# Kernel tuning notes

Measured on AMD Instinct MI355X. Metric: run time of the kernel, lower is better.

Reference implementation:

```python
import jax, jax.numpy as jnp
import numpy as np

NC, S, T, F, D, A = 617, 200000, 15, 5, 64, 768
E, EC, L = 1000000, 20000, 2


def setup_inputs():
    key = jax.random.key(0)
    ks = jax.random.split(key, 24)
    f = jnp.float32
    sc = 0.08
    return {
        "company_ts": jax.random.normal(ks[0], (NC, T, F), f),
        "sentence_x": jax.random.normal(ks[1], (S, A), f),
        "company_ids": jnp.arange(NC, dtype=jnp.int32),
        "ei_c2c_src": jax.random.randint(ks[2], (EC,), 0, NC),
        "ei_c2c_dst": jax.random.randint(ks[3], (EC,), 0, NC),
        "ei_s2c_src": jax.random.randint(ks[4], (E,), 0, S),
        "ei_s2c_dst": jax.random.randint(ks[5], (E,), 0, NC),
        "ei_c2s_src": jax.random.randint(ks[6], (E,), 0, NC),
        "ei_c2s_dst": jax.random.randint(ks[7], (E,), 0, S),
        "bn_gamma": jnp.ones((T,), f),
        "bn_beta": jnp.zeros((T,), f),
        "lstm_Wih0": sc * jax.random.normal(ks[8], (4 * D, 1), f),
        "lstm_Whh0": sc * jax.random.normal(ks[9], (4 * D, D), f),
        "lstm_bih0": jnp.zeros((4 * D,), f),
        "lstm_bhh0": jnp.zeros((4 * D,), f),
        "lstm_Wih1": sc * jax.random.normal(ks[10], (4 * D, D), f),
        "lstm_Whh1": sc * jax.random.normal(ks[11], (4 * D, D), f),
        "lstm_bih1": jnp.zeros((4 * D,), f),
        "lstm_bhh1": jnp.zeros((4 * D,), f),
        "fc_W": sc * jax.random.normal(ks[12], (D, D), f),
        "fc_b": jnp.zeros((D,), f),
        "comp_emb": jax.random.normal(ks[13], (NC, D), f),
        "proj_W": sc * jax.random.normal(ks[14], (D, A), f),
        "proj_b": jnp.zeros((D,), f),
        "gin_W": sc * jax.random.normal(ks[15], (L, 3, D, D), f),
        "gin_b": jnp.zeros((L, 3, D), f),
        "gin_a": 0.25 * jnp.ones((L, 3), f),  # PReLU slope, torch default init
        "cls_W": sc * jax.random.normal(ks[16], (2, D), f),
        "cls_b": jnp.zeros((2,), f),
    }


def _lstm_layer(x, Wih, Whh, bih, bhh):
    # x: [N, T, I] -> [N, T, H]; torch gate order i, f, g, o
    N = x.shape[0]
    H = Whh.shape[1]

    def step(carry, xt):
        h, c = carry
        g = xt @ Wih.T + h @ Whh.T + bih + bhh
        i, fg, gg, o = jnp.split(g, 4, axis=-1)
        c = jax.nn.sigmoid(fg) * c + jax.nn.sigmoid(i) * jnp.tanh(gg)
        h = jax.nn.sigmoid(o) * jnp.tanh(c)
        return (h, c), h

    init = (jnp.zeros((N, H), x.dtype), jnp.zeros((N, H), x.dtype))
    _, hs = jax.lax.scan(step, init, jnp.swapaxes(x, 0, 1))
    return jnp.swapaxes(hs, 0, 1)


def _gin(x_src, x_dst, src, dst, n_dst, W, b, a):
    # GINConv(eps=0), nn = Linear + PReLU: prelu(W @ (x_dst + sum_{e->i} x_src[src_e]) + b)
    msg = jax.ops.segment_sum(x_src[src], dst, num_segments=n_dst)
    h = (x_dst + msg) @ W.T + b
    return jnp.where(h >= 0, h, a * h)


def reference(company_ts, sentence_x, company_ids, ei_c2c_src, ei_c2c_dst,
              ei_s2c_src, ei_s2c_dst, ei_c2s_src, ei_c2s_dst,
              bn_gamma, bn_beta, lstm_Wih0, lstm_Whh0, lstm_bih0, lstm_bhh0,
              lstm_Wih1, lstm_Whh1, lstm_bih1, lstm_bhh1, fc_W, fc_b,
              comp_emb, proj_W, proj_b, gin_W, gin_b, gin_a, cls_W, cls_b):
    # LSTM branch on the second-to-last timeseries feature
    ts = company_ts[:, :, -2:-1]                       # [NC, T, 1]
    mean = ts.mean(axis=(0, 2), keepdims=True)         # BatchNorm1d(T), training stats
    var = ts.var(axis=(0, 2), keepdims=True)
    ts = (ts - mean) / jnp.sqrt(var + 1e-5)
    ts = ts * bn_gamma[None, :, None] + bn_beta[None, :, None]
    h = _lstm_layer(ts, lstm_Wih0, lstm_Whh0, lstm_bih0, lstm_bhh0)
    h = _lstm_layer(h, lstm_Wih1, lstm_Whh1, lstm_bih1, lstm_bhh1)
    comp_ts = jax.nn.relu(h[:, -1, :] @ fc_W.T + fc_b)  # [NC, D]

    # node features: company = lstm + embedding; sentence = projected article emb
    comp = comp_ts + comp_emb[company_ids]
    sent = sentence_x @ proj_W.T + proj_b               # [S, D]

    # to_hetero(GConv): per-edge-type GINConv, sum-aggregate over edge types per dst type
    n_comp, n_sent = comp.shape[0], sent.shape[0]
    for l in range(gin_W.shape[0]):
        new_comp = (_gin(comp, comp, ei_c2c_src, ei_c2c_dst, n_comp,
                         gin_W[l, 0], gin_b[l, 0], gin_a[l, 0])
                    + _gin(sent, comp, ei_s2c_src, ei_s2c_dst, n_comp,
                           gin_W[l, 1], gin_b[l, 1], gin_a[l, 1]))
        new_sent = _gin(comp, sent, ei_c2s_src, ei_c2s_dst, n_sent,
                        gin_W[l, 2], gin_b[l, 2], gin_a[l, 2])
        comp, sent = new_comp, new_sent

    return comp @ cls_W.T + cls_b                       # [NC, 2]
```

## Files before the change

kernel.cpp:

```cpp
#include <hip/hip_runtime.h>

#define NCC 617
#define TTT 15
#define FFF 5
#define SSN 200000
#define EEN 1000000
#define ECN 20000
#define CSBLK 196
#define NB2 512
#define EPB2 ((EEN + NB2 - 1) / NB2)
#define ZN (NCC + NCC + SSN + SSN)
#define HALLB ((ECN + EEN + 255) / 256)
#define SGB 782

typedef unsigned short u16;
typedef unsigned int   u32;

using short8  = __attribute__((ext_vector_type(8))) short;
using f32x4v  = __attribute__((ext_vector_type(4))) float;

__device__ __forceinline__ float bf2f(u16 u){ return __uint_as_float(((u32)u) << 16); }
__device__ __forceinline__ u16 f2bf(float f){
  u32 x = __float_as_uint(f);
  u32 r = (x + 0x7fffu + ((x >> 16) & 1u)) >> 16;
  return (u16)r;
}
__device__ __forceinline__ u32 pk2(float a, float b){ return (u32)f2bf(a) | ((u32)f2bf(b) << 16); }
__device__ __forceinline__ float sigm(float x){ return 1.0f / (1.0f + __expf(-x)); }

__global__ __launch_bounds__(256) void k_zero(int* p, int n){
  int i = blockIdx.x * 256 + threadIdx.x;
  if (i < n) p[i] = 0;
}

__global__ __launch_bounds__(256) void k_histF(const int* __restrict__ s2c_dst, int* __restrict__ blockHist,
                                               const int* __restrict__ c2c_dst, int* __restrict__ cnt_c2c,
                                               const int* __restrict__ c2s_dst, int* __restrict__ cnt_c2s){
  __shared__ int h[NCC];
  int b = blockIdx.x, tid = threadIdx.x;
  if (b < NB2){
    for (int i = tid; i < NCC; i += 256) h[i] = 0;
    __syncthreads();
    int e0 = b * EPB2;
    int e1 = e0 + EPB2; if (e1 > EEN) e1 = EEN;
    for (int e = e0 + tid; e < e1; e += 256) atomicAdd(&h[s2c_dst[e]], 1);
    __syncthreads();
    for (int i = tid; i < NCC; i += 256) blockHist[i * NB2 + b] = h[i];
  } else {
    int i = (b - NB2) * 256 + tid;
    if (i < ECN) atomicAdd(&cnt_c2c[c2c_dst[i]], 1);
    else if (i < ECN + EEN) atomicAdd(&cnt_c2s[c2s_dst[i - ECN]], 1);
  }
}

__global__ __launch_bounds__(1024) void k_scanA(int* __restrict__ blockHist, int* __restrict__ colTotal,
                                                const int* __restrict__ cnt_c2s, int* __restrict__ off_c2s,
                                                int* __restrict__ bsum,
                                                const float* __restrict__ ts, const float* __restrict__ gamma,
                                                const float* __restrict__ beta, float* __restrict__ tsn){
  __shared__ int buf[1024];
  __shared__ float ss[1024], s2[1024];
  int b = blockIdx.x, tid = threadIdx.x;
  if (b < NCC){
    if (tid < 64){
      int lane = tid;
      int base = 0;
      for (int j = 0; j < NB2; j += 64){
        int v = blockHist[b * NB2 + j + lane];
        int orig = v;
        #pragma unroll
        for (int s = 1; s < 64; s <<= 1){
          int t = __shfl_up(v, s, 64);
          if (lane >= s) v += t;
        }
        blockHist[b * NB2 + j + lane] = base + v - orig;
        base += __shfl(v, 63, 64);
      }
      if (lane == 0) colTotal[b] = base;
    }
  } else if (b < NCC + CSBLK) {
    int bb = b - NCC;
    int gi = bb * 1024 + tid;
    int v = (gi < SSN) ? cnt_c2s[gi] : 0;
    buf[tid] = v;
    __syncthreads();
    for (int d = 1; d < 1024; d <<= 1){
      int x = (tid >= d) ? buf[tid - d] : 0;
      __syncthreads();
      buf[tid] += x;
      __syncthreads();
    }
    if (gi < SSN) off_c2s[gi] = buf[tid] - v;
    if (tid == 1023) bsum[bb] = buf[1023];
  } else {
    int t = b - (NCC + CSBLK);
    float a = 0.f, s = 0.f;
    for (int c = tid; c < NCC; c += 1024){
      float v = ts[(c * TTT + t) * FFF + 3];
      a += v; s += v * v;
    }
    ss[tid] = a; s2[tid] = s;
    __syncthreads();
    for (int d = 512; d > 0; d >>= 1){
      if (tid < d){ ss[tid] += ss[tid + d]; s2[tid] += s2[tid + d]; }
      __syncthreads();
    }
    float mean = ss[0] / (float)NCC;
    float var  = s2[0] / (float)NCC - mean * mean;
    float rstd = rsqrtf(var + 1e-5f);
    float g = gamma[t], be = beta[t];
    for (int c = tid; c < NCC; c += 1024){
      float v = ts[(c * TTT + t) * FFF + 3];
      tsn[c * TTT + t] = (v - mean) * rstd * g + be;
    }
  }
}

__global__ __launch_bounds__(1024) void k_scanB(const int* __restrict__ cnt_c2c, int* __restrict__ off_c2c,
                                                const int* __restrict__ colTotal, int* __restrict__ off_s2c,
                                                int* __restrict__ off_c2s, const int* __restrict__ bsum){
  __shared__ int buf[1024];
  __shared__ int sboff[CSBLK + 1];
  int b = blockIdx.x, tid = threadIdx.x;
  if (b == 0){
    for (int pass = 0; pass < 2; ++pass){
      const int* cnt = pass ? colTotal : cnt_c2c;
      int* ofs = pass ? off_s2c : off_c2c;
      int v = (tid < NCC) ? cnt[tid] : 0;
      buf[tid] = v;
      __syncthreads();
      for (int d = 1; d < 1024; d <<= 1){
        int x = (tid >= d) ? buf[tid - d] : 0;
        __syncthreads();
        buf[tid] += x;
        __syncthreads();
      }
      if (tid < NCC) ofs[tid] = (tid == 0) ? 0 : buf[tid - 1];
      if (tid == 0) ofs[NCC] = buf[NCC - 1];
      __syncthreads();
    }
  } else {
    int bb = b - 1;
    int lane = tid & 63;
    if (tid < 64){
      int base = 0;
      for (int j = 0; j < CSBLK; j += 64){
        int idx = j + lane;
        int v = (idx < CSBLK) ? bsum[idx] : 0;
        int orig = v;
        #pragma unroll
        for (int s = 1; s < 64; s <<= 1){
          int t2 = __shfl_up(v, s, 64);
          if (lane >= s) v += t2;
        }
        if (idx < CSBLK) sboff[idx] = base + v - orig;
        base += __shfl(v, 63, 64);
      }
      if (lane == 0) sboff[CSBLK] = base;
    }
    __syncthreads();
    int gi = bb * 1024 + tid;
    if (gi < SSN) off_c2s[gi] += sboff[bb];
    if (bb == 0 && tid == 0) off_c2s[SSN] = sboff[CSBLK];
  }
}

__global__ __launch_bounds__(256) void k_scatF(const int* __restrict__ s2c_src, const int* __restrict__ s2c_dst,
                                               const int* __restrict__ blockHist, const int* __restrict__ off_s2c,
                                               int* __restrict__ bkt_s2c,
                                               const int* __restrict__ c2c_src, const int* __restrict__ c2c_dst,
                                               const int* __restrict__ off_c2c, int* __restrict__ cnt2_c2c,
                                               int* __restrict__ bkt_c2c,
                                               const int* __restrict__ c2s_src, const int* __restrict__ c2s_dst,
                                               const int* __restrict__ off_c2s, int* __restrict__ cnt2_c2s,
                                               int* __restrict__ bkt_c2s){
  __shared__ int cur[NCC];
  int b = blockIdx.x, tid = threadIdx.x;
  if (b < NB2){
    for (int i = tid; i < NCC; i += 256) cur[i] = off_s2c[i] + blockHist[i * NB2 + b];
    __syncthreads();
    int e0 = b * EPB2;
    int e1 = e0 + EPB2; if (e1 > EEN) e1 = EEN;
    for (int e = e0 + tid; e < e1; e += 256){
      int d = s2c_dst[e];
      int p = atomicAdd(&cur[d], 1);
      bkt_s2c[p] = s2c_src[e];
    }
  } else {
    int i = (b - NB2) * 256 + tid;
    if (i < ECN){
      int d = c2c_dst[i]; int p = off_c2c[d] + atomicAdd(&cnt2_c2c[d], 1); bkt_c2c[p] = c2c_src[i];
    } else if (i < ECN + EEN){
      int k = i - ECN;
      int d = c2s_dst[k]; int p = off_c2s[d] + atomicAdd(&cnt2_c2s[d], 1); bkt_c2s[p] = c2s_src[k];
    }
  }
}

__global__ __launch_bounds__(256, 1) void k_lstm01(const float* __restrict__ tsn,
                                                   const float* __restrict__ Wih0, const float* __restrict__ Whh0,
                                                   const float* __restrict__ bih0, const float* __restrict__ bhh0,
                                                   const float* __restrict__ Wih1, const float* __restrict__ Whh1,
                                                   const float* __restrict__ bih1, const float* __restrict__ bhh1,
                                                   const float* __restrict__ fcW, const float* __restrict__ fcb,
                                                   const float* __restrict__ emb, const int* __restrict__ ids,
                                                   float* __restrict__ comp0){
  __shared__ __align__(16) u16 sW0[64 * 64 * 4];
  __shared__ __align__(16) u16 sP1[64 * 64 * 8];
  __shared__ float sWi[256];
  __shared__ float sB0[256];
  int tid = threadIdx.x;
  for (int i = tid; i < 16384; i += 256){
    int k = i >> 8, j = (i >> 2) & 63, g = i & 3;
    sW0[i] = f2bf(Whh0[(g * 64 + j) * 64 + k]);
  }
  for (int i = tid; i < 32768; i += 256){
    int k = i >> 9, j = (i >> 3) & 63, g = i & 7;
    float v = (g < 4) ? Wih1[(g * 64 + j) * 64 + k] : Whh1[((g - 4) * 64 + j) * 64 + k];
    sP1[i] = f2bf(v);
  }
  sWi[tid] = Wih0[tid];
  sB0[tid] = bih0[tid] + bhh0[tid];
  __syncthreads();
  int wave = tid >> 6, lane = tid & 63;
  int c = blockIdx.x * 4 + wave;
  int ci = (c < NCC) ? c : (NCC - 1);
  float wi_i = sWi[lane], wi_f = sWi[64 + lane], wi_g = sWi[128 + lane], wi_o = sWi[192 + lane];
  float b0i = sB0[lane], b0f = sB0[64 + lane], b0g = sB0[128 + lane], b0o = sB0[192 + lane];
  float b1i = bih1[lane]       + bhh1[lane];
  float b1f = bih1[64 + lane]  + bhh1[64 + lane];
  float b1g = bih1[128 + lane] + bhh1[128 + lane];
  float b1o = bih1[192 + lane] + bhh1[192 + lane];
  float h0 = 0.f, c0 = 0.f, h1 = 0.f, c1 = 0.f;
  for (int t = 0; t < TTT; ++t){
    float x = tsn[ci * TTT + t];
    float gi = b0i + x * wi_i, gf = b0f + x * wi_f, gg = b0g + x * wi_g, go = b0o + x * wi_o;
    #pragma unroll 4
    for (int k = 0; k < 64; ++k){
      float hk = __shfl(h0, k, 64);
      ushort4 w = *(const ushort4*)&sW0[(k * 64 + lane) * 4];
      gi += hk * bf2f(w.x); gf += hk * bf2f(w.y);
      gg += hk * bf2f(w.z); go += hk * bf2f(w.w);
    }
    c0 = sigm(gf) * c0 + sigm(gi) * tanhf(gg);
    h0 = sigm(go) * tanhf(c0);
    gi = b1i; gf = b1f; gg = b1g; go = b1o;
    #pragma unroll 4
    for (int k = 0; k < 64; ++k){
      float xk = __shfl(h0, k, 64);
      float hk = __shfl(h1, k, 64);
      short8 wv = *(const short8*)&sP1[(k * 64 + lane) * 8];
      gi += xk * bf2f((u16)wv[0]) + hk * bf2f((u16)wv[4]);
      gf += xk * bf2f((u16)wv[1]) + hk * bf2f((u16)wv[5]);
      gg += xk * bf2f((u16)wv[2]) + hk * bf2f((u16)wv[6]);
      go += xk * bf2f((u16)wv[3]) + hk * bf2f((u16)wv[7]);
    }
    c1 = sigm(gf) * c1 + sigm(gi) * tanhf(gg);
    h1 = sigm(go) * tanhf(c1);
  }
  __syncthreads();
  float* fws = (float*)sW0;
  for (int i = tid; i < 4096; i += 256){
    int d = i >> 6, k = i & 63;
    fws[k * 64 + d] = fcW[i];
  }
  __syncthreads();
  float y = fcb[lane];
  #pragma unroll 4
  for (int k = 0; k < 64; ++k){
    float hk = __shfl(h1, k, 64);
    y += hk * fws[k * 64 + lane];
  }
  y = fmaxf(y, 0.f);
  if (c < NCC) comp0[c * 64 + lane] = y + emb[ids[c] * 64 + lane];
}

__global__ __launch_bounds__(256) void k_projm(const float* __restrict__ A, const float* __restrict__ W,
                                               const float* __restrict__ pb, u16* __restrict__ sent0){
  __shared__ __align__(16) u16 sA[128 * 64];
  __shared__ __align__(16) u16 sB[64 * 64];
  char* sAb = (char*)sA;
  char* sBb = (char*)sB;
  int tid = threadIdx.x;
  int wave = tid >> 6, lane = tid & 63;
  int l15 = lane & 15, lg = lane >> 4;
  int s0 = blockIdx.x * 128;

  int rA = tid >> 1, hA = tid & 1;
  int sA_row = s0 + rA; if (sA_row >= SSN) sA_row = SSN - 1;
  const float* gA0 = &A[(size_t)sA_row * 768 + hA * 32];
  u32 aw_base = (u32)(rA * 128 + hA * 64);
  u32 aw_swz  = (u32)((rA & 7) << 4);
  int nB = tid >> 2, qB = tid & 3;
  const float* gB0 = &W[(size_t)nB * 768 + qB * 16];
  u32 bw_base = (u32)(nB * 128 + qB * 32);
  u32 bw_swz  = (u32)((nB & 7) << 4);

  int arow = wave * 32 + l15;
  u32 ar_swz = (u32)((arow & 7) << 4);
  u32 ar_base = (u32)(arow * 128 + lg * 16);
  u32 br_swz = (u32)((l15 & 7) << 4);
  u32 br_base = (u32)(l15 * 128 + lg * 16);

  f32x4v acc[2][4] = {};

  for (int kc = 0; kc < 12; ++kc){
    __syncthreads();
    {
      const float* g = gA0 + kc * 64;
      #pragma unroll
      for (int q = 0; q < 4; ++q){
        float4 va = ((const float4*)g)[2 * q];
        float4 vb = ((const float4*)g)[2 * q + 1];
        uint4 w;
        w.x = pk2(va.x, va.y); w.y = pk2(va.z, va.w);
        w.z = pk2(vb.x, vb.y); w.w = pk2(vb.z, vb.w);
        *(uint4*)(sAb + ((aw_base + q * 16) ^ aw_swz)) = w;
      }
    }
    {
      const float* g = gB0 + kc * 64;
      #pragma unroll
      for (int q = 0; q < 2; ++q){
        float4 va = ((const float4*)g)[2 * q];
        float4 vb = ((const float4*)g)[2 * q + 1];
        uint4 w;
        w.x = pk2(va.x, va.y); w.y = pk2(va.z, va.w);
        w.z = pk2(vb.x, vb.y); w.w = pk2(vb.z, vb.w);
        *(uint4*)(sBb + ((bw_base + q * 16) ^ bw_swz)) = w;
      }
    }
    __syncthreads();
    #pragma unroll
    for (int ks = 0; ks < 2; ++ks){
      short8 a0 = *(const short8*)(sAb + ((ar_base + 0    + ks * 64) ^ ar_swz));
      short8 a1 = *(const short8*)(sAb + ((ar_base + 2048 + ks * 64) ^ ar_swz));
      short8 b0 = *(const short8*)(sBb + ((br_base + 0    + ks * 64) ^ br_swz));
      short8 b1 = *(const short8*)(sBb + ((br_base + 2048 + ks * 64) ^ br_swz));
      short8 b2 = *(const short8*)(sBb + ((br_base + 4096 + ks * 64) ^ br_swz));
      short8 b3 = *(const short8*)(sBb + ((br_base + 6144 + ks * 64) ^ br_swz));
      acc[0][0] = __builtin_amdgcn_mfma_f32_16x16x32_bf16(a0, b0, acc[0][0], 0, 0, 0);
      acc[0][1] = __builtin_amdgcn_mfma_f32_16x16x32_bf16(a0, b1, acc[0][1], 0, 0, 0);
      acc[0][2] = __builtin_amdgcn_mfma_f32_16x16x32_bf16(a0, b2, acc[0][2], 0, 0, 0);
      acc[0][3] = __builtin_amdgcn_mfma_f32_16x16x32_bf16(a0, b3, acc[0][3], 0, 0, 0);
      acc[1][0] = __builtin_amdgcn_mfma_f32_16x16x32_bf16(a1, b0, acc[1][0], 0, 0, 0);
      acc[1][1] = __builtin_amdgcn_mfma_f32_16x16x32_bf16(a1, b1, acc[1][1], 0, 0, 0);
      acc[1][2] = __builtin_amdgcn_mfma_f32_16x16x32_bf16(a1, b2, acc[1][2], 0, 0, 0);
      acc[1][3] = __builtin_amdgcn_mfma_f32_16x16x32_bf16(a1, b3, acc[1][3], 0, 0, 0);
    }
  }

  float bias[4];
  #pragma unroll
  for (int nt = 0; nt < 4; ++nt) bias[nt] = pb[nt * 16 + l15];
  #pragma unroll
  for (int mt = 0; mt < 2; ++mt){
    #pragma unroll
    for (int j = 0; j < 4; ++j){
      int s = s0 + wave * 32 + mt * 16 + lg * 4 + j;
      if (s < SSN){
        #pragma unroll
        for (int nt = 0; nt < 4; ++nt)
          sent0[(size_t)s * 64 + nt * 16 + l15] = f2bf(acc[mt][nt][j] + bias[nt]);
      }
    }
  }
}

__global__ __launch_bounds__(1024) void k_gin0(const float* __restrict__ compIn, const u16* __restrict__ sentIn,
                                               const int* __restrict__ ofsA, const int* __restrict__ bktA,
                                               const int* __restrict__ ofsB, const int* __restrict__ bktB,
                                               const int* __restrict__ ofsS, const int* __restrict__ bktS,
                                               const float* __restrict__ gin_W, const float* __restrict__ gin_b,
                                               const float* __restrict__ gin_a,
                                               float* __restrict__ compOut, u16* __restrict__ sentOut){
  __shared__ __align__(16) char smem[52224];
  int tid = threadIdx.x;
  int wave = tid >> 6, lane = tid & 63;
  int b = blockIdx.x;
  if (b < NCC){
    float* Wat  = (float*)smem;
    float* Wbt  = Wat + 64 * 68;
    int*   eidx = (int*)(Wbt + 64 * 68);
    float* part = (float*)(eidx + 2048);
    float* xa   = part + 2048;
    float* xb   = xa + 64;
    float* outab = xb + 64;
    const float* Wa = gin_W + 0 * 4096;
    const float* Wb = gin_W + 1 * 4096;
    for (int i = tid; i < 4096; i += 1024){
      int j = i >> 6, k = i & 63;
      Wat[k * 68 + j] = Wa[i];
      Wbt[k * 68 + j] = Wb[i];
    }
    int c = b;
    float accA = 0.f, accB = 0.f;
    int a0 = ofsA[c], a1 = ofsA[c + 1];
    for (int base = a0; base < a1; base += 2048){
      int cnt = a1 - base; if (cnt > 2048) cnt = 2048;
      __syncthreads();
      for (int i = tid; i < cnt; i += 1024) eidx[i] = bktA[base + i];
      __syncthreads();
      #pragma unroll 4
      for (int i = wave; i < cnt; i += 16) accA += compIn[eidx[i] * 64 + lane];
    }
    int b0 = ofsB[c], b1 = ofsB[c + 1];
    for (int base = b0; base < b1; base += 2048){
      int cnt = b1 - base; if (cnt > 2048) cnt = 2048;
      __syncthreads();
      for (int i = tid; i < cnt; i += 1024) eidx[i] = bktB[base + i];
      __syncthreads();
      #pragma unroll 8
      for (int i = wave; i < cnt; i += 16) accB += bf2f(sentIn[(size_t)eidx[i] * 64 + lane]);
    }
    part[(wave * 2 + 0) * 64 + lane] = accA;
    part[(wave * 2 + 1) * 64 + lane] = accB;
    __syncthreads();
    if (tid < 128){
      int l = tid & 63, which = tid >> 6;
      float m = 0.f;
      #pragma unroll
      for (int w = 0; w < 16; ++w) m += part[(w * 2 + which) * 64 + l];
      float ci = compIn[c * 64 + l];
      if (which == 0) xa[l] = ci + m; else xb[l] = ci + m;
    }
    __syncthreads();
    if (tid < 128){
      int j = tid & 63;
      const float* X  = (tid < 64) ? xa : xb;
      const float* Wt = (tid < 64) ? Wat : Wbt;
      float acc = (tid < 64) ? gin_b[j] : gin_b[64 + j];
      #pragma unroll 4
      for (int k = 0; k < 64; ++k) acc += X[k] * Wt[k * 68 + j];
      float al = (tid < 64) ? gin_a[0] : gin_a[1];
      outab[tid] = (acc >= 0.f) ? acc : al * acc;
    }
    __syncthreads();
    if (tid < 64) compOut[c * 64 + tid] = outab[tid] + outab[64 + tid];
  } else {
    u16* sX   = (u16*)smem;
    u16* sW   = sX + 16384;
    int* eb   = (int*)(sW + 4096);
    int* sofs = eb + 2048;
    char* sXb = (char*)sX;
    char* sWb = (char*)sW;
    const float* W = gin_W + 2 * 4096;
    const float* bi = gin_b + 128;
    {
      int n = tid >> 4, q = tid & 15;
      float4 v = *(const float4*)&W[n * 64 + q * 4];
      uint2 w;
      w.x = pk2(v.x, v.y); w.y = pk2(v.z, v.w);
      *(uint2*)(sWb + (((u32)(n * 128 + q * 8)) ^ ((u32)((n & 7) << 4)))) = w;
    }
    int sBase = (b - NCC) * 256;
    if (tid < 257){
      int idx = sBase + tid; if (idx > SSN) idx = SSN;
      sofs[tid] = ofsS[idx];
    }
    __syncthreads();
    int E0 = sofs[0];
    int tot = sofs[256] - E0;
    int staged = tot < 2048 ? tot : 2048;
    for (int i = tid; i < staged; i += 1024) eb[i] = bktS[E0 + i];
    __syncthreads();
    for (int q = 0; q < 16; ++q){
      int sL = wave * 16 + q;
      int s = sBase + sL;
      if (s < SSN){
        float acc = bf2f(sentIn[(size_t)s * 64 + lane]);
        int e0 = sofs[sL], e1 = sofs[sL + 1];
        for (int e = e0; e < e1; ++e){
          int r = e - E0;
          int src = (r < 2048) ? eb[r] : bktS[e];
          acc += compIn[src * 64 + lane];
        }
        *(u16*)(sXb + (((u32)(sL * 128 + lane * 2)) ^ ((u32)((sL & 7) << 4)))) = f2bf(acc);
      }
    }
    __syncthreads();
    int l15 = lane & 15, lg = lane >> 4;
    int arow = wave * 16 + l15;
    u32 ar_swz = (u32)((arow & 7) << 4);
    u32 br_swz = (u32)((l15 & 7) << 4);
    f32x4v acc4[4] = {};
    #pragma unroll
    for (int ks = 0; ks < 2; ++ks){
      short8 a0 = *(const short8*)(sXb + (((u32)(arow * 128 + ks * 64 + lg * 16)) ^ ar_swz));
      #pragma unroll
      for (int nt = 0; nt < 4; ++nt){
        short8 b0 = *(const short8*)(sWb + (((u32)((nt * 16 + l15) * 128 + ks * 64 + lg * 16)) ^ br_swz));
        acc4[nt] = __builtin_amdgcn_mfma_f32_16x16x32_bf16(a0, b0, acc4[nt], 0, 0, 0);
      }
    }
    float alpha = gin_a[2];
    #pragma unroll
    for (int nt = 0; nt < 4; ++nt){
      float bb = bi[nt * 16 + l15];
      #pragma unroll
      for (int j = 0; j < 4; ++j){
        int srow = sBase + wave * 16 + lg * 4 + j;
        if (srow < SSN){
          float h = acc4[nt][j] + bb;
          h = (h >= 0.f) ? h : alpha * h;
          sentOut[(size_t)srow * 64 + nt * 16 + l15] = f2bf(h);
        }
      }
    }
  }
}

__global__ __launch_bounds__(1024) void k_cgin1(const float* __restrict__ compIn, const u16* __restrict__ sentIn,
                                                const int* __restrict__ ofsA, const int* __restrict__ bktA,
                                                const int* __restrict__ ofsB, const int* __restrict__ bktB,
                                                const float* __restrict__ Wa, const float* __restrict__ ba, const float* aaP,
                                                const float* __restrict__ Wb, const float* __restrict__ bb, const float* abP,
                                                const float* __restrict__ clsW, const float* __restrict__ clsb,
                                                float* __restrict__ outp){
  __shared__ __align__(16) float Wat[64 * 68];
  __shared__ __align__(16) float Wbt[64 * 68];
  __shared__ int eidx[2048];
  __shared__ float part[16][2][64];
  __shared__ float xa[64], xb[64], outab[128];
  int tid = threadIdx.x;
  for (int i = tid; i < 4096; i += 1024){
    int j = i >> 6, k = i & 63;
    Wat[k * 68 + j] = Wa[i];
    Wbt[k * 68 + j] = Wb[i];
  }
  int wave = tid >> 6, lane = tid & 63;
  int c = blockIdx.x;
  float accA = 0.f, accB = 0.f;
  int a0 = ofsA[c], a1 = ofsA[c + 1];
  for (int base = a0; base < a1; base += 2048){
    int cnt = a1 - base; if (cnt > 2048) cnt = 2048;
    __syncthreads();
    for (int i = tid; i < cnt; i += 1024) eidx[i] = bktA[base + i];
    __syncthreads();
    #pragma unroll 4
    for (int i = wave; i < cnt; i += 16) accA += compIn[eidx[i] * 64 + lane];
  }
  int b0 = ofsB[c], b1 = ofsB[c + 1];
  for (int base = b0; base < b1; base += 2048){
    int cnt = b1 - base; if (cnt > 2048) cnt = 2048;
    __syncthreads();
    for (int i = tid; i < cnt; i += 1024) eidx[i] = bktB[base + i];
    __syncthreads();
    #pragma unroll 8
    for (int i = wave; i < cnt; i += 16) accB += bf2f(sentIn[(size_t)eidx[i] * 64 + lane]);
  }
  part[wave][0][lane] = accA;
  part[wave][1][lane] = accB;
  __syncthreads();
  if (tid < 128){
    int l = tid & 63, which = tid >> 6;
    float m = 0.f;
    #pragma unroll
    for (int w = 0; w < 16; ++w) m += part[w][which][l];
    float ci = compIn[c * 64 + l];
    if (which == 0) xa[l] = ci + m; else xb[l] = ci + m;
  }
  __syncthreads();
  if (tid < 128){
    int j = tid & 63;
    const float* X  = (tid < 64) ? xa : xb;
    const float* Wt = (tid < 64) ? Wat : Wbt;
    float acc = (tid < 64) ? ba[j] : bb[j];
    #pragma unroll 4
    for (int k = 0; k < 64; ++k) acc += X[k] * Wt[k * 68 + j];
    float al = (tid < 64) ? *aaP : *abP;
    outab[tid] = (acc >= 0.f) ? acc : al * acc;
  }
  __syncthreads();
  if (tid < 64) xa[tid] = outab[tid] + outab[64 + tid];
  __syncthreads();
  if (tid < 128){
    int j = tid >> 6;
    float p = xa[lane] * clsW[j * 64 + lane];
    #pragma unroll
    for (int s = 32; s > 0; s >>= 1) p += __shfl_down(p, s, 64);
    if (lane == 0) outp[c * 2 + j] = p + clsb[j];
  }
}

extern "C" void kernel_launch(void* const* d_in, const int* in_sizes, int n_in,
                              void* d_out, int out_size, void* d_ws, size_t ws_size,
                              hipStream_t stream) {
  (void)in_sizes; (void)n_in; (void)out_size; (void)ws_size;
  const float* company_ts = (const float*)d_in[0];
  const float* sentence_x = (const float*)d_in[1];
  const int*   company_ids = (const int*)d_in[2];
  const int*   c2c_src = (const int*)d_in[3];
  const int*   c2c_dst = (const int*)d_in[4];
  const int*   s2c_src = (const int*)d_in[5];
  const int*   s2c_dst = (const int*)d_in[6];
  const int*   c2s_src = (const int*)d_in[7];
  const int*   c2s_dst = (const int*)d_in[8];
  const float* bn_gamma = (const float*)d_in[9];
  const float* bn_beta  = (const float*)d_in[10];
  const float* Wih0 = (const float*)d_in[11];
  const float* Whh0 = (const float*)d_in[12];
  const float* bih0 = (const float*)d_in[13];
  const float* bhh0 = (const float*)d_in[14];
  const float* Wih1 = (const float*)d_in[15];
  const float* Whh1 = (const float*)d_in[16];
  const float* bih1 = (const float*)d_in[17];
  const float* bhh1 = (const float*)d_in[18];
  const float* fc_W = (const float*)d_in[19];
  const float* fc_b = (const float*)d_in[20];
  const float* comp_emb = (const float*)d_in[21];
  const float* proj_W = (const float*)d_in[22];
  const float* proj_b = (const float*)d_in[23];
  const float* gin_W = (const float*)d_in[24];
  const float* gin_b = (const float*)d_in[25];
  const float* gin_a = (const float*)d_in[26];
  const float* cls_W = (const float*)d_in[27];
  const float* cls_b = (const float*)d_in[28];
  float* outp = (float*)d_out;

  char* ws = (char*)d_ws;
  size_t off = 0;
  auto alloc = [&](size_t bytes)->char* {
    char* r = ws + off;
    off += (bytes + 255) & ~(size_t)255;
    return r;
  };
  float* ts_norm = (float*)alloc((size_t)NCC * TTT * 4);
  float* comp0   = (float*)alloc((size_t)NCC * 64 * 4);
  float* comp1   = (float*)alloc((size_t)NCC * 64 * 4);
  u16*   sent0   = (u16*)alloc((size_t)SSN * 64 * 2);
  u16*   sent1   = (u16*)alloc((size_t)SSN * 64 * 2);
  int*   blockHist = (int*)alloc((size_t)NCC * NB2 * 4);
  int*   colTotal  = (int*)alloc((size_t)NCC * 4);
  int*   cnt_c2c  = (int*)alloc((size_t)ZN * 4);
  int*   cnt2_c2c = cnt_c2c + NCC;
  int*   cnt_c2s  = cnt2_c2c + NCC;
  int*   cnt2_c2s = cnt_c2s + SSN;
  int*   off_c2c = (int*)alloc((size_t)(NCC + 1) * 4);
  int*   off_s2c = (int*)alloc((size_t)(NCC + 1) * 4);
  int*   off_c2s = (int*)alloc((size_t)(SSN + 1) * 4);
  int*   bkt_c2c = (int*)alloc((size_t)ECN * 4);
  int*   bkt_s2c = (int*)alloc((size_t)EEN * 4);
  int*   bkt_c2s = (int*)alloc((size_t)EEN * 4);
  int*   bsum    = (int*)alloc(256 * 4);

  k_zero<<<(ZN + 255) / 256, 256, 0, stream>>>(cnt_c2c, ZN);
  k_histF<<<NB2 + HALLB, 256, 0, stream>>>(s2c_dst, blockHist, c2c_dst, cnt_c2c, c2s_dst, cnt_c2s);
  k_scanA<<<NCC + CSBLK + TTT, 1024, 0, stream>>>(blockHist, colTotal, cnt_c2s, off_c2s, bsum,
                                                  company_ts, bn_gamma, bn_beta, ts_norm);
  k_scanB<<<1 + CSBLK, 1024, 0, stream>>>(cnt_c2c, off_c2c, colTotal, off_s2c, off_c2s, bsum);
  k_scatF<<<NB2 + HALLB, 256, 0, stream>>>(s2c_src, s2c_dst, blockHist, off_s2c, bkt_s2c,
                                           c2c_src, c2c_dst, off_c2c, cnt2_c2c, bkt_c2c,
                                           c2s_src, c2s_dst, off_c2s, cnt2_c2s, bkt_c2s);

  k_lstm01<<<(NCC + 3) / 4, 256, 0, stream>>>(ts_norm, Wih0, Whh0, bih0, bhh0,
                                              Wih1, Whh1, bih1, bhh1,
                                              fc_W, fc_b, comp_emb, company_ids, comp0);

  k_projm<<<(SSN + 127) / 128, 256, 0, stream>>>(sentence_x, proj_W, proj_b, sent0);

  k_gin0<<<NCC + SGB, 1024, 0, stream>>>(comp0, sent0,
                                         off_c2c, bkt_c2c, off_s2c, bkt_s2c,
                                         off_c2s, bkt_c2s,
                                         gin_W, gin_b, gin_a,
                                         comp1, sent1);

  k_cgin1<<<NCC, 1024, 0, stream>>>(comp1, sent1,
                                    off_c2c, bkt_c2c, off_s2c, bkt_s2c,
                                    gin_W + 3 * 4096, gin_b + 3 * 64, gin_a + 3,
                                    gin_W + 4 * 4096, gin_b + 4 * 64, gin_a + 4,
                                    cls_W, cls_b, outp);
}
```

Before: 552.5 us.

## Merge projection GEMM into histogram kernel and LSTM into scan kernel

The sentence projection GEMM now runs as extra blocks of the histogram kernel, and the LSTM runs as extra blocks of the second scan kernel, using 16 companies per 1024-thread block instead of 4 per 256-thread block. The zeroing kernel is replaced by hipMemsetAsync. The aim is to cut launch count and let independent work overlap within one grid. In exchange, the LSTM blocks need about 100KB of shared memory, which the scan blocks also reserve, and the much larger block size cuts the number of LSTM blocks and may lower occupancy.

```diff
diff --git a/kernel.cpp b/kernel.cpp
--- a/kernel.cpp
+++ b/kernel.cpp
@@ -12,6 +12,8 @@
 #define ZN (NCC + NCC + SSN + SSN)
 #define HALLB ((ECN + EEN + 255) / 256)
 #define SGB 782
+#define PROJB ((SSN + 127) / 128)
+#define LSTMB ((NCC + 15) / 16)
 
 typedef unsigned short u16;
 typedef unsigned int   u32;
@@ -28,26 +30,113 @@
 __device__ __forceinline__ u32 pk2(float a, float b){ return (u32)f2bf(a) | ((u32)f2bf(b) << 16); }
 __device__ __forceinline__ float sigm(float x){ return 1.0f / (1.0f + __expf(-x)); }
 
-__global__ __launch_bounds__(256) void k_zero(int* p, int n){
-  int i = blockIdx.x * 256 + threadIdx.x;
-  if (i < n) p[i] = 0;
-}
-
-__global__ __launch_bounds__(256) void k_histF(const int* __restrict__ s2c_dst, int* __restrict__ blockHist,
-                                               const int* __restrict__ c2c_dst, int* __restrict__ cnt_c2c,
-                                               const int* __restrict__ c2s_dst, int* __restrict__ cnt_c2s){
+__global__ __launch_bounds__(256) void k_histproj(const float* __restrict__ A, const float* __restrict__ W,
+                                                  const float* __restrict__ pb, u16* __restrict__ sent0,
+                                                  const int* __restrict__ s2c_dst, int* __restrict__ blockHist,
+                                                  const int* __restrict__ c2c_dst, int* __restrict__ cnt_c2c,
+                                                  const int* __restrict__ c2s_dst, int* __restrict__ cnt_c2s){
+  __shared__ __align__(16) u16 sA[128 * 64];
+  __shared__ __align__(16) u16 sB[64 * 64];
   __shared__ int h[NCC];
-  int b = blockIdx.x, tid = threadIdx.x;
-  if (b < NB2){
+  int tid = threadIdx.x;
+  int b = blockIdx.x;
+  if (b < PROJB){
+    char* sAb = (char*)sA;
+    char* sBb = (char*)sB;
+    int wave = tid >> 6, lane = tid & 63;
+    int l15 = lane & 15, lg = lane >> 4;
+    int s0 = b * 128;
+
+    int rA = tid >> 1, hA = tid & 1;
+    int sA_row = s0 + rA; if (sA_row >= SSN) sA_row = SSN - 1;
+    const float* gA0 = &A[(size_t)sA_row * 768 + hA * 32];
+    u32 aw_base = (u32)(rA * 128 + hA * 64);
+    u32 aw_swz  = (u32)((rA & 7) << 4);
+    int nB = tid >> 2, qB = tid & 3;
+    const float* gB0 = &W[(size_t)nB * 768 + qB * 16];
+    u32 bw_base = (u32)(nB * 128 + qB * 32);
+    u32 bw_swz  = (u32)((nB & 7) << 4);
+
+    int arow = wave * 32 + l15;
+    u32 ar_swz = (u32)((arow & 7) << 4);
+    u32 ar_base = (u32)(arow * 128 + lg * 16);
+    u32 br_swz = (u32)((l15 & 7) << 4);
+    u32 br_base = (u32)(l15 * 128 + lg * 16);
+
+    f32x4v acc[2][4] = {};
+
+    for (int kc = 0; kc < 12; ++kc){
+      __syncthreads();
+      {
+        const float* g = gA0 + kc * 64;
+        #pragma unroll
+        for (int q = 0; q < 4; ++q){
+          float4 va = ((const float4*)g)[2 * q];
+          float4 vb = ((const float4*)g)[2 * q + 1];
+          uint4 w;
+          w.x = pk2(va.x, va.y); w.y = pk2(va.z, va.w);
+          w.z = pk2(vb.x, vb.y); w.w = pk2(vb.z, vb.w);
+          *(uint4*)(sAb + ((aw_base + q * 16) ^ aw_swz)) = w;
+        }
+      }
+      {
+        const float* g = gB0 + kc * 64;
+        #pragma unroll
+        for (int q = 0; q < 2; ++q){
+          float4 va = ((const float4*)g)[2 * q];
+          float4 vb = ((const float4*)g)[2 * q + 1];
+          uint4 w;
+          w.x = pk2(va.x, va.y); w.y = pk2(va.z, va.w);
+          w.z = pk2(vb.x, vb.y); w.w = pk2(vb.z, vb.w);
+          *(uint4*)(sBb + ((bw_base + q * 16) ^ bw_swz)) = w;
+        }
+      }
+      __syncthreads();
+      #pragma unroll
+      for (int ks = 0; ks < 2; ++ks){
+        short8 a0 = *(const short8*)(sAb + ((ar_base + 0    + ks * 64) ^ ar_swz));
+        short8 a1 = *(const short8*)(sAb + ((ar_base + 2048 + ks * 64) ^ ar_swz));
+        short8 b0 = *(const short8*)(sBb + ((br_base + 0    + ks * 64) ^ br_swz));
+        short8 b1 = *(const short8*)(sBb + ((br_base + 2048 + ks * 64) ^ br_swz));
+        short8 b2 = *(const short8*)(sBb + ((br_base + 4096 + ks * 64) ^ br_swz));
+        short8 b3 = *(const short8*)(sBb + ((br_base + 6144 + ks * 64) ^ br_swz));
+        acc[0][0] = __builtin_amdgcn_mfma_f32_16x16x32_bf16(a0, b0, acc[0][0], 0, 0, 0);
+        acc[0][1] = __builtin_amdgcn_mfma_f32_16x16x32_bf16(a0, b1, acc[0][1], 0, 0, 0);
+        acc[0][2] = __builtin_amdgcn_mfma_f32_16x16x32_bf16(a0, b2, acc[0][2], 0, 0, 0);
+        acc[0][3] = __builtin_amdgcn_mfma_f32_16x16x32_bf16(a0, b3, acc[0][3], 0, 0, 0);
+        acc[1][0] = __builtin_amdgcn_mfma_f32_16x16x32_bf16(a1, b0, acc[1][0], 0, 0, 0);
+        acc[1][1] = __builtin_amdgcn_mfma_f32_16x16x32_bf16(a1, b1, acc[1][1], 0, 0, 0);
+        acc[1][2] = __builtin_amdgcn_mfma_f32_16x16x32_bf16(a1, b2, acc[1][2], 0, 0, 0);
+        acc[1][3] = __builtin_amdgcn_mfma_f32_16x16x32_bf16(a1, b3, acc[1][3], 0, 0, 0);
+      }
+    }
+
+    float bias[4];
+    #pragma unroll
+    for (int nt = 0; nt < 4; ++nt) bias[nt] = pb[nt * 16 + l15];
+    #pragma unroll
+    for (int mt = 0; mt < 2; ++mt){
+      #pragma unroll
+      for (int j = 0; j < 4; ++j){
+        int s = s0 + wave * 32 + mt * 16 + lg * 4 + j;
+        if (s < SSN){
+          #pragma unroll
+          for (int nt = 0; nt < 4; ++nt)
+            sent0[(size_t)s * 64 + nt * 16 + l15] = f2bf(acc[mt][nt][j] + bias[nt]);
+        }
+      }
+    }
+  } else if (b < PROJB + NB2){
+    int bb = b - PROJB;
     for (int i = tid; i < NCC; i += 256) h[i] = 0;
     __syncthreads();
-    int e0 = b * EPB2;
+    int e0 = bb * EPB2;
     int e1 = e0 + EPB2; if (e1 > EEN) e1 = EEN;
     for (int e = e0 + tid; e < e1; e += 256) atomicAdd(&h[s2c_dst[e]], 1);
     __syncthreads();
-    for (int i = tid; i < NCC; i += 256) blockHist[i * NB2 + b] = h[i];
+    for (int i = tid; i < NCC; i += 256) blockHist[i * NB2 + bb] = h[i];
   } else {
-    int i = (b - NB2) * 256 + tid;
+    int i = (b - PROJB - NB2) * 256 + tid;
     if (i < ECN) atomicAdd(&cnt_c2c[c2c_dst[i]], 1);
     else if (i < ECN + EEN) atomicAdd(&cnt_c2s[c2s_dst[i - ECN]], 1);
   }
@@ -116,13 +205,24 @@
   }
 }
 
-__global__ __launch_bounds__(1024) void k_scanB(const int* __restrict__ cnt_c2c, int* __restrict__ off_c2c,
-                                                const int* __restrict__ colTotal, int* __restrict__ off_s2c,
-                                                int* __restrict__ off_c2s, const int* __restrict__ bsum){
-  __shared__ int buf[1024];
-  __shared__ int sboff[CSBLK + 1];
+__global__ __launch_bounds__(1024) void k_scanBL(const int* __restrict__ cnt_c2c, int* __restrict__ off_c2c,
+                                                 const int* __restrict__ colTotal, int* __restrict__ off_s2c,
+                                                 int* __restrict__ off_c2s, const int* __restrict__ bsum,
+                                                 const float* __restrict__ tsn,
+                                                 const float* __restrict__ Wih0, const float* __restrict__ Whh0,
+                                                 const float* __restrict__ bih0, const float* __restrict__ bhh0,
+                                                 const float* __restrict__ Wih1, const float* __restrict__ Whh1,
+                                                 const float* __restrict__ bih1, const float* __restrict__ bhh1,
+                                                 const float* __restrict__ fcW, const float* __restrict__ fcb,
+                                                 const float* __restrict__ emb, const int* __restrict__ ids,
+                                                 float* __restrict__ comp0){
+  __shared__ __align__(16) u16 sW0[64 * 64 * 4];
+  __shared__ __align__(16) u16 sP1[64 * 64 * 8];
+  __shared__ float sWi[256];
+  __shared__ float sB0[256];
   int b = blockIdx.x, tid = threadIdx.x;
   if (b == 0){
+    int* buf = (int*)sW0;
     for (int pass = 0; pass < 2; ++pass){
       const int* cnt = pass ? colTotal : cnt_c2c;
       int* ofs = pass ? off_s2c : off_c2c;
@@ -139,7 +239,8 @@
       if (tid == 0) ofs[NCC] = buf[NCC - 1];
       __syncthreads();
     }
-  } else {
+  } else if (b <= CSBLK){
+    int* sboff = (int*)sW0;
     int bb = b - 1;
     int lane = tid & 63;
     if (tid < 64){
@@ -162,6 +263,73 @@
     int gi = bb * 1024 + tid;
     if (gi < SSN) off_c2s[gi] += sboff[bb];
     if (bb == 0 && tid == 0) off_c2s[SSN] = sboff[CSBLK];
+  } else {
+    int bb = b - (CSBLK + 1);
+    for (int i = tid; i < 16384; i += 1024){
+      int k = i >> 8, j = (i >> 2) & 63, g = i & 3;
+      sW0[i] = f2bf(Whh0[(g * 64 + j) * 64 + k]);
+    }
+    for (int i = tid; i < 32768; i += 1024){
+      int k = i >> 9, j = (i >> 3) & 63, g = i & 7;
+      float v = (g < 4) ? Wih1[(g * 64 + j) * 64 + k] : Whh1[((g - 4) * 64 + j) * 64 + k];
+      sP1[i] = f2bf(v);
+    }
+    if (tid < 256){
+      sWi[tid] = Wih0[tid];
+      sB0[tid] = bih0[tid] + bhh0[tid];
+    }
+    __syncthreads();
+    int wave = tid >> 6, lane = tid & 63;
+    int c = bb * 16 + wave;
+    int ci = (c < NCC) ? c : (NCC - 1);
+    float wi_i = sWi[lane], wi_f = sWi[64 + lane], wi_g = sWi[128 + lane], wi_o = sWi[192 + lane];
+    float b0i = sB0[lane], b0f = sB0[64 + lane], b0g = sB0[128 + lane], b0o = sB0[192 + lane];
+    float b1i = bih1[lane]       + bhh1[lane];
+    float b1f = bih1[64 + lane]  + bhh1[64 + lane];
+    float b1g = bih1[128 + lane] + bhh1[128 + lane];
+    float b1o = bih1[192 + lane] + bhh1[192 + lane];
+    float h0 = 0.f, c0 = 0.f, h1 = 0.f, c1 = 0.f;
+    for (int t = 0; t < TTT; ++t){
+      float x = tsn[ci * TTT + t];
+      float gi = b0i + x * wi_i, gf = b0f + x * wi_f, gg = b0g + x * wi_g, go = b0o + x * wi_o;
+      #pragma unroll 4
+      for (int k = 0; k < 64; ++k){
+        float hk = __shfl(h0, k, 64);
+        ushort4 w = *(const ushort4*)&sW0[(k * 64 + lane) * 4];
+        gi += hk * bf2f(w.x); gf += hk * bf2f(w.y);
+        gg += hk * bf2f(w.z); go += hk * bf2f(w.w);
+      }
+      c0 = sigm(gf) * c0 + sigm(gi) * tanhf(gg);
+      h0 = sigm(go) * tanhf(c0);
+      gi = b1i; gf = b1f; gg = b1g; go = b1o;
+      #pragma unroll 4
+      for (int k = 0; k < 64; ++k){
+        float xk = __shfl(h0, k, 64);
+        float hk = __shfl(h1, k, 64);
+        short8 wv = *(const short8*)&sP1[(k * 64 + lane) * 8];
+        gi += xk * bf2f((u16)wv[0]) + hk * bf2f((u16)wv[4]);
+        gf += xk * bf2f((u16)wv[1]) + hk * bf2f((u16)wv[5]);
+        gg += xk * bf2f((u16)wv[2]) + hk * bf2f((u16)wv[6]);
+        go += xk * bf2f((u16)wv[3]) + hk * bf2f((u16)wv[7]);
+      }
+      c1 = sigm(gf) * c1 + sigm(gi) * tanhf(gg);
+      h1 = sigm(go) * tanhf(c1);
+    }
+    __syncthreads();
+    float* fws = (float*)sW0;
+    for (int i = tid; i < 4096; i += 1024){
+      int d = i >> 6, k = i & 63;
+      fws[k * 64 + d] = fcW[i];
+    }
+    __syncthreads();
+    float y = fcb[lane];
+    #pragma unroll 4
+    for (int k = 0; k < 64; ++k){
+      float hk = __shfl(h1, k, 64);
+      y += hk * fws[k * 64 + lane];
+    }
+    y = fmaxf(y, 0.f);
+    if (c < NCC) comp0[c * 64 + lane] = y + emb[ids[c] * 64 + lane];
   }
 }
 
@@ -193,176 +361,6 @@
     } else if (i < ECN + EEN){
       int k = i - ECN;
       int d = c2s_dst[k]; int p = off_c2s[d] + atomicAdd(&cnt2_c2s[d], 1); bkt_c2s[p] = c2s_src[k];
-    }
-  }
-}
-
-__global__ __launch_bounds__(256, 1) void k_lstm01(const float* __restrict__ tsn,
-                                                   const float* __restrict__ Wih0, const float* __restrict__ Whh0,
-                                                   const float* __restrict__ bih0, const float* __restrict__ bhh0,
-                                                   const float* __restrict__ Wih1, const float* __restrict__ Whh1,
-                                                   const float* __restrict__ bih1, const float* __restrict__ bhh1,
-                                                   const float* __restrict__ fcW, const float* __restrict__ fcb,
-                                                   const float* __restrict__ emb, const int* __restrict__ ids,
-                                                   float* __restrict__ comp0){
-  __shared__ __align__(16) u16 sW0[64 * 64 * 4];
-  __shared__ __align__(16) u16 sP1[64 * 64 * 8];
-  __shared__ float sWi[256];
-  __shared__ float sB0[256];
-  int tid = threadIdx.x;
-  for (int i = tid; i < 16384; i += 256){
-    int k = i >> 8, j = (i >> 2) & 63, g = i & 3;
-    sW0[i] = f2bf(Whh0[(g * 64 + j) * 64 + k]);
-  }
-  for (int i = tid; i < 32768; i += 256){
-    int k = i >> 9, j = (i >> 3) & 63, g = i & 7;
-    float v = (g < 4) ? Wih1[(g * 64 + j) * 64 + k] : Whh1[((g - 4) * 64 + j) * 64 + k];
-    sP1[i] = f2bf(v);
-  }
-  sWi[tid] = Wih0[tid];
-  sB0[tid] = bih0[tid] + bhh0[tid];
-  __syncthreads();
-  int wave = tid >> 6, lane = tid & 63;
-  int c = blockIdx.x * 4 + wave;
-  int ci = (c < NCC) ? c : (NCC - 1);
-  float wi_i = sWi[lane], wi_f = sWi[64 + lane], wi_g = sWi[128 + lane], wi_o = sWi[192 + lane];
-  float b0i = sB0[lane], b0f = sB0[64 + lane], b0g = sB0[128 + lane], b0o = sB0[192 + lane];
-  float b1i = bih1[lane]       + bhh1[lane];
-  float b1f = bih1[64 + lane]  + bhh1[64 + lane];
-  float b1g = bih1[128 + lane] + bhh1[128 + lane];
-  float b1o = bih1[192 + lane] + bhh1[192 + lane];
-  float h0 = 0.f, c0 = 0.f, h1 = 0.f, c1 = 0.f;
-  for (int t = 0; t < TTT; ++t){
-    float x = tsn[ci * TTT + t];
-    float gi = b0i + x * wi_i, gf = b0f + x * wi_f, gg = b0g + x * wi_g, go = b0o + x * wi_o;
-    #pragma unroll 4
-    for (int k = 0; k < 64; ++k){
-      float hk = __shfl(h0, k, 64);
-      ushort4 w = *(const ushort4*)&sW0[(k * 64 + lane) * 4];
-      gi += hk * bf2f(w.x); gf += hk * bf2f(w.y);
-      gg += hk * bf2f(w.z); go += hk * bf2f(w.w);
-    }
-    c0 = sigm(gf) * c0 + sigm(gi) * tanhf(gg);
-    h0 = sigm(go) * tanhf(c0);
-    gi = b1i; gf = b1f; gg = b1g; go = b1o;
-    #pragma unroll 4
-    for (int k = 0; k < 64; ++k){
-      float xk = __shfl(h0, k, 64);
-      float hk = __shfl(h1, k, 64);
-      short8 wv = *(const short8*)&sP1[(k * 64 + lane) * 8];
-      gi += xk * bf2f((u16)wv[0]) + hk * bf2f((u16)wv[4]);
-      gf += xk * bf2f((u16)wv[1]) + hk * bf2f((u16)wv[5]);
-      gg += xk * bf2f((u16)wv[2]) + hk * bf2f((u16)wv[6]);
-      go += xk * bf2f((u16)wv[3]) + hk * bf2f((u16)wv[7]);
-    }
-    c1 = sigm(gf) * c1 + sigm(gi) * tanhf(gg);
-    h1 = sigm(go) * tanhf(c1);
-  }
-  __syncthreads();
-  float* fws = (float*)sW0;
-  for (int i = tid; i < 4096; i += 256){
-    int d = i >> 6, k = i & 63;
-    fws[k * 64 + d] = fcW[i];
-  }
-  __syncthreads();
-  float y = fcb[lane];
-  #pragma unroll 4
-  for (int k = 0; k < 64; ++k){
-    float hk = __shfl(h1, k, 64);
-    y += hk * fws[k * 64 + lane];
-  }
-  y = fmaxf(y, 0.f);
-  if (c < NCC) comp0[c * 64 + lane] = y + emb[ids[c] * 64 + lane];
-}
-
-__global__ __launch_bounds__(256) void k_projm(const float* __restrict__ A, const float* __restrict__ W,
-                                               const float* __restrict__ pb, u16* __restrict__ sent0){
-  __shared__ __align__(16) u16 sA[128 * 64];
-  __shared__ __align__(16) u16 sB[64 * 64];
-  char* sAb = (char*)sA;
-  char* sBb = (char*)sB;
-  int tid = threadIdx.x;
-  int wave = tid >> 6, lane = tid & 63;
-  int l15 = lane & 15, lg = lane >> 4;
-  int s0 = blockIdx.x * 128;
-
-  int rA = tid >> 1, hA = tid & 1;
-  int sA_row = s0 + rA; if (sA_row >= SSN) sA_row = SSN - 1;
-  const float* gA0 = &A[(size_t)sA_row * 768 + hA * 32];
-  u32 aw_base = (u32)(rA * 128 + hA * 64);
-  u32 aw_swz  = (u32)((rA & 7) << 4);
-  int nB = tid >> 2, qB = tid & 3;
-  const float* gB0 = &W[(size_t)nB * 768 + qB * 16];
-  u32 bw_base = (u32)(nB * 128 + qB * 32);
-  u32 bw_swz  = (u32)((nB & 7) << 4);
-
-  int arow = wave * 32 + l15;
-  u32 ar_swz = (u32)((arow & 7) << 4);
-  u32 ar_base = (u32)(arow * 128 + lg * 16);
-  u32 br_swz = (u32)((l15 & 7) << 4);
-  u32 br_base = (u32)(l15 * 128 + lg * 16);
-
-  f32x4v acc[2][4] = {};
-
-  for (int kc = 0; kc < 12; ++kc){
-    __syncthreads();
-    {
-      const float* g = gA0 + kc * 64;
-      #pragma unroll
-      for (int q = 0; q < 4; ++q){
-        float4 va = ((const float4*)g)[2 * q];
-        float4 vb = ((const float4*)g)[2 * q + 1];
-        uint4 w;
-        w.x = pk2(va.x, va.y); w.y = pk2(va.z, va.w);
-        w.z = pk2(vb.x, vb.y); w.w = pk2(vb.z, vb.w);
-        *(uint4*)(sAb + ((aw_base + q * 16) ^ aw_swz)) = w;
-      }
-    }
-    {
-      const float* g = gB0 + kc * 64;
-      #pragma unroll
-      for (int q = 0; q < 2; ++q){
-        float4 va = ((const float4*)g)[2 * q];
-        float4 vb = ((const float4*)g)[2 * q + 1];
-        uint4 w;
-        w.x = pk2(va.x, va.y); w.y = pk2(va.z, va.w);
-        w.z = pk2(vb.x, vb.y); w.w = pk2(vb.z, vb.w);
-        *(uint4*)(sBb + ((bw_base + q * 16) ^ bw_swz)) = w;
-      }
-    }
-    __syncthreads();
-    #pragma unroll
-    for (int ks = 0; ks < 2; ++ks){
-      short8 a0 = *(const short8*)(sAb + ((ar_base + 0    + ks * 64) ^ ar_swz));
-      short8 a1 = *(const short8*)(sAb + ((ar_base + 2048 + ks * 64) ^ ar_swz));
-      short8 b0 = *(const short8*)(sBb + ((br_base + 0    + ks * 64) ^ br_swz));
-      short8 b1 = *(const short8*)(sBb + ((br_base + 2048 + ks * 64) ^ br_swz));
-      short8 b2 = *(const short8*)(sBb + ((br_base + 4096 + ks * 64) ^ br_swz));
-      short8 b3 = *(const short8*)(sBb + ((br_base + 6144 + ks * 64) ^ br_swz));
-      acc[0][0] = __builtin_amdgcn_mfma_f32_16x16x32_bf16(a0, b0, acc[0][0], 0, 0, 0);
-      acc[0][1] = __builtin_amdgcn_mfma_f32_16x16x32_bf16(a0, b1, acc[0][1], 0, 0, 0);
-      acc[0][2] = __builtin_amdgcn_mfma_f32_16x16x32_bf16(a0, b2, acc[0][2], 0, 0, 0);
-      acc[0][3] = __builtin_amdgcn_mfma_f32_16x16x32_bf16(a0, b3, acc[0][3], 0, 0, 0);
-      acc[1][0] = __builtin_amdgcn_mfma_f32_16x16x32_bf16(a1, b0, acc[1][0], 0, 0, 0);
-      acc[1][1] = __builtin_amdgcn_mfma_f32_16x16x32_bf16(a1, b1, acc[1][1], 0, 0, 0);
-      acc[1][2] = __builtin_amdgcn_mfma_f32_16x16x32_bf16(a1, b2, acc[1][2], 0, 0, 0);
-      acc[1][3] = __builtin_amdgcn_mfma_f32_16x16x32_bf16(a1, b3, acc[1][3], 0, 0, 0);
-    }
-  }
-
-  float bias[4];
-  #pragma unroll
-  for (int nt = 0; nt < 4; ++nt) bias[nt] = pb[nt * 16 + l15];
-  #pragma unroll
-  for (int mt = 0; mt < 2; ++mt){
-    #pragma unroll
-    for (int j = 0; j < 4; ++j){
-      int s = s0 + wave * 32 + mt * 16 + lg * 4 + j;
-      if (s < SSN){
-        #pragma unroll
-        for (int nt = 0; nt < 4; ++nt)
-          sent0[(size_t)s * 64 + nt * 16 + l15] = f2bf(acc[mt][nt][j] + bias[nt]);
-      }
     }
   }
 }
@@ -644,20 +642,23 @@
   int*   bkt_c2s = (int*)alloc((size_t)EEN * 4);
   int*   bsum    = (int*)alloc(256 * 4);
 
-  k_zero<<<(ZN + 255) / 256, 256, 0, stream>>>(cnt_c2c, ZN);
-  k_histF<<<NB2 + HALLB, 256, 0, stream>>>(s2c_dst, blockHist, c2c_dst, cnt_c2c, c2s_dst, cnt_c2s);
+  hipMemsetAsync(cnt_c2c, 0, (size_t)ZN * 4, stream);
+
+  k_histproj<<<PROJB + NB2 + HALLB, 256, 0, stream>>>(sentence_x, proj_W, proj_b, sent0,
+                                                      s2c_dst, blockHist, c2c_dst, cnt_c2c,
+                                                      c2s_dst, cnt_c2s);
+
   k_scanA<<<NCC + CSBLK + TTT, 1024, 0, stream>>>(blockHist, colTotal, cnt_c2s, off_c2s, bsum,
                                                   company_ts, bn_gamma, bn_beta, ts_norm);
-  k_scanB<<<1 + CSBLK, 1024, 0, stream>>>(cnt_c2c, off_c2c, colTotal, off_s2c, off_c2s, bsum);
+
+  k_scanBL<<<1 + CSBLK + LSTMB, 1024, 0, stream>>>(cnt_c2c, off_c2c, colTotal, off_s2c, off_c2s, bsum,
+                                                   ts_norm, Wih0, Whh0, bih0, bhh0,
+                                                   Wih1, Whh1, bih1, bhh1,
+                                                   fc_W, fc_b, comp_emb, company_ids, comp0);
+
   k_scatF<<<NB2 + HALLB, 256, 0, stream>>>(s2c_src, s2c_dst, blockHist, off_s2c, bkt_s2c,
                                            c2c_src, c2c_dst, off_c2c, cnt2_c2c, bkt_c2c,
                                            c2s_src, c2s_dst, off_c2s, cnt2_c2s, bkt_c2s);
-
-  k_lstm01<<<(NCC + 3) / 4, 256, 0, stream>>>(ts_norm, Wih0, Whh0, bih0, bhh0,
-                                              Wih1, Whh1, bih1, bhh1,
-                                              fc_W, fc_b, comp_emb, company_ids, comp0);
-
-  k_projm<<<(SSN + 127) / 128, 256, 0, stream>>>(sentence_x, proj_W, proj_b, sent0);
 
   k_gin0<<<NCC + SGB, 1024, 0, stream>>>(comp0, sent0,
                                          off_c2c, bkt_c2c, off_s2c, bkt_s2c,
```

Result: slower. 625.0 us (+13.1%).
